# Performance work log

Measured on AMD Instinct MI355X. Metric: run time of the kernel, lower is better.

## Reference

```python
import jax, jax.numpy as jnp
import numpy as np

N_NODES = 100000
DROP_P = 0.2


def _degree_norm(idx, n):
    deg = jax.ops.segment_sum(jnp.ones_like(idx, dtype=jnp.float32), idx, num_segments=n)
    return jnp.maximum(deg, 1.0) ** -0.5


def gcn_layer(x, src, dst, W, b, n):
    # DGL GraphConv, norm='both', in_feats > out_feats so weight is applied first.
    norm_src = _degree_norm(src, n)  # out-degree^{-1/2}
    norm_dst = _degree_norm(dst, n)  # in-degree^{-1/2}
    h = (x * norm_src[:, None]) @ W            # [N, d_out]
    agg = jax.ops.segment_sum(h[src], dst, num_segments=n)  # gather-scatter over edges
    return agg * norm_dst[:, None] + b


def setup_inputs() -> dict:
    key = jax.random.key(0)
    k = jax.random.split(key, 5)
    x = jax.random.normal(k[0], (N_NODES, 256), dtype=jnp.float32)
    edge_index = jax.random.randint(k[1], (2, 1600000), 0, N_NODES, dtype=jnp.int64)
    W1 = jax.random.normal(k[2], (256, 128), dtype=jnp.float32) * (1.0 / np.sqrt(256))
    b1 = jnp.zeros((128,), dtype=jnp.float32)
    W2 = jax.random.normal(k[3], (128, 47), dtype=jnp.float32) * (1.0 / np.sqrt(128))
    b2 = jnp.zeros((47,), dtype=jnp.float32)
    return {"x": x, "edge_index": edge_index, "W1": W1, "b1": b1, "W2": W2, "b2": b2}


def reference(x, edge_index, W1, b1, W2, b2):
    src, dst = edge_index[0], edge_index[1]
    n = x.shape[0]
    # CRD: GraphConv -> relu -> dropout (F.dropout default training=True; fixed mask)
    h = gcn_layer(x, src, dst, W1, b1, n)
    h = jax.nn.relu(h)
    keep = jax.random.bernoulli(jax.random.key(42), 1.0 - DROP_P, h.shape)
    h = jnp.where(keep, h / (1.0 - DROP_P), 0.0)
    # CLS: GraphConv -> log_softmax over class dim
    out = gcn_layer(h, src, dst, W2, b2, n)
    return jax.nn.log_softmax(out, axis=-1)
```

## Files before the change

### kernel.cpp

```cpp
#include <hip/hip_runtime.h>
#include <math.h>


#define NF0 256
#define NF1 128
#define NC  47
#define CB  1024

typedef __attribute__((ext_vector_type(8))) short bfrag;
typedef __attribute__((ext_vector_type(4))) float f32x4;

__device__ __forceinline__ unsigned short f2bf(float f) {
  unsigned u = __float_as_uint(f);
  return (unsigned short)((u + 0x7fffu + ((u >> 16) & 1u)) >> 16);
}
__device__ __forceinline__ unsigned pack2bf(float a, float b) {
  return (unsigned)f2bf(a) | ((unsigned)f2bf(b) << 16);
}
__device__ __forceinline__ float bflo(unsigned v) { return __uint_as_float(v << 16); }
__device__ __forceinline__ float bfhi(unsigned v) { return __uint_as_float(v & 0xffff0000u); }
__device__ __forceinline__ float bf2f(unsigned short b) {
  return __uint_as_float((unsigned)b << 16);
}

__device__ __forceinline__ unsigned rotl_(unsigned x, int n) {
  return (x << n) | (x >> (32 - n));
}
__device__ __forceinline__ void threefry2x32_(unsigned x0, unsigned x1,
                                              unsigned& o0, unsigned& o1) {
  const unsigned k0 = 0u, k1 = 42u;
  const unsigned k2 = k0 ^ k1 ^ 0x1BD11BDAu;
  x0 += k0; x1 += k1;
  x0+=x1; x1=rotl_(x1,13); x1^=x0;
  x0+=x1; x1=rotl_(x1,15); x1^=x0;
  x0+=x1; x1=rotl_(x1,26); x1^=x0;
  x0+=x1; x1=rotl_(x1, 6); x1^=x0;
  x0+=k1; x1+=k2+1u;
  x0+=x1; x1=rotl_(x1,17); x1^=x0;
  x0+=x1; x1=rotl_(x1,29); x1^=x0;
  x0+=x1; x1=rotl_(x1,16); x1^=x0;
  x0+=x1; x1=rotl_(x1,24); x1^=x0;
  x0+=k2; x1+=k0+2u;
  x0+=x1; x1=rotl_(x1,13); x1^=x0;
  x0+=x1; x1=rotl_(x1,15); x1^=x0;
  x0+=x1; x1=rotl_(x1,26); x1^=x0;
  x0+=x1; x1=rotl_(x1, 6); x1^=x0;
  x0+=k0; x1+=k1+3u;
  x0+=x1; x1=rotl_(x1,17); x1^=x0;
  x0+=x1; x1=rotl_(x1,29); x1^=x0;
  x0+=x1; x1=rotl_(x1,16); x1^=x0;
  x0+=x1; x1=rotl_(x1,24); x1^=x0;
  x0+=k1; x1+=k2+4u;
  x0+=x1; x1=rotl_(x1,13); x1^=x0;
  x0+=x1; x1=rotl_(x1,15); x1^=x0;
  x0+=x1; x1=rotl_(x1,26); x1^=x0;
  x0+=x1; x1=rotl_(x1, 6); x1^=x0;
  x0+=k2; x1+=k0+5u;
  o0 = x0; o1 = x1;
}
__device__ __forceinline__ unsigned dropout_bit(unsigned j) {
  unsigned o0, o1;
  threefry2x32_(0u, j, o0, o1);
  unsigned bits = o0 ^ o1;
  float u = __uint_as_float((bits >> 9) | 0x3f800000u) - 1.0f;
  return (u < 0.8f) ? 1u : 0u;
}


__global__ __launch_bounds__(256) void k_chist(const int* __restrict__ ei, int E,
                                               int nbk,
                                               unsigned* __restrict__ bCntD,
                                               unsigned* __restrict__ bCntS,
                                               const float* __restrict__ W1,
                                               const float* __restrict__ W2,
                                               unsigned* __restrict__ W1t32,
                                               unsigned* __restrict__ W2t32) {
  if (blockIdx.x >= 256) {
    int i = (blockIdx.x - 256) * 256 + threadIdx.x;
    if (i < 128 * 128) {
      int n = i >> 7, k = (i & 127) << 1;
      W1t32[i] = pack2bf(W1[(size_t)k * NF1 + n], W1[(size_t)(k + 1) * NF1 + n]);
    } else if (i < 128 * 128 + 48 * 64) {
      int j = i - 128 * 128;
      int f = j >> 6, k = (j & 63) << 1;
      float a = (f < NC) ? W2[(size_t)k * NC + f] : 0.f;
      float c = (f < NC) ? W2[(size_t)(k + 1) * NC + f] : 0.f;
      W2t32[j] = pack2bf(a, c);
    }
    return;
  }
  __shared__ unsigned hd[128], hs[128];
  for (int i = threadIdx.x; i < 128; i += 256) { hd[i] = 0; hs[i] = 0; }
  __syncthreads();
  for (int e = blockIdx.x * 256 + threadIdx.x; e < E; e += 256 * 256) {
    int s = ei[e], d = ei[E + e];
    atomicAdd(&hs[s >> 10], 1u);
    atomicAdd(&hd[d >> 10], 1u);
  }
  __syncthreads();
  for (int i = threadIdx.x; i < nbk; i += 256) {
    if (hd[i]) atomicAdd(&bCntD[i], hd[i]);
    if (hs[i]) atomicAdd(&bCntS[i], hs[i]);
  }
}

__global__ __launch_bounds__(256) void k_cscatter(const int* __restrict__ ei, int E,
                                                  const unsigned* __restrict__ bCntD,
                                                  const unsigned* __restrict__ bCntS,
                                                  unsigned* __restrict__ curD,
                                                  unsigned* __restrict__ curS,
                                                  unsigned* __restrict__ pd,
                                                  unsigned short* __restrict__ ps,
                                                  int nbk) {
  __shared__ unsigned hd[128], hs[128];
  __shared__ unsigned baseD[128], baseS[128];
  __shared__ unsigned sc[256];
  const int t = threadIdx.x;
  int per = (E + gridDim.x - 1) / gridDim.x;
  int e0 = blockIdx.x * per;
  int e1 = min(e0 + per, E);
  unsigned orig = (t < 128) ? ((t < nbk) ? bCntD[t] : 0u)
                            : (((t - 128) < nbk) ? bCntS[t - 128] : 0u);
  sc[t] = orig;
  if (t < 128) { hd[t] = 0; hs[t] = 0; }
  __syncthreads();
  for (int e = e0 + t; e < e1; e += 256) {
    int s = ei[e], d = ei[E + e];
    atomicAdd(&hs[s >> 10], 1u);
    atomicAdd(&hd[d >> 10], 1u);
  }
  __syncthreads();
  #pragma unroll
  for (int o = 1; o < 128; o <<= 1) {
    unsigned u = ((t & 127) >= o) ? sc[t - o] : 0u;
    __syncthreads();
    sc[t] += u;
    __syncthreads();
  }
  if (t < 128) {
    unsigned excl = sc[t] - orig;
    unsigned h = hd[t];
    baseD[t] = excl + (h ? atomicAdd(&curD[t], h) : 0u);
    hd[t] = 0;
  } else {
    int i = t - 128;
    unsigned excl = sc[t] - orig;
    unsigned h = hs[i];
    baseS[i] = excl + (h ? atomicAdd(&curS[i], h) : 0u);
    hs[i] = 0;
  }
  __syncthreads();
  for (int e = e0 + t; e < e1; e += 256) {
    int s = ei[e], d = ei[E + e];
    int bd = d >> 10, bs = s >> 10;
    unsigned pD = baseD[bd] + atomicAdd(&hd[bd], 1u);
    unsigned pS = baseS[bs] + atomicAdd(&hs[bs], 1u);
    pd[pD] = ((unsigned)(d & (CB - 1)) << 17) | (unsigned)s;
    ps[pS] = (unsigned short)(s & (CB - 1));
  }
}

__global__ __launch_bounds__(256) void k_fine(const unsigned* __restrict__ bCntD,
                                              const unsigned* __restrict__ bCntS,
                                              const unsigned* __restrict__ pd,
                                              const unsigned short* __restrict__ ps,
                                              unsigned* __restrict__ off,
                                              float* __restrict__ norm_dst,
                                              float* __restrict__ norm_src,
                                              int* __restrict__ csr,
                                              int N, int E, int nbk,
                                              unsigned* __restrict__ bmask) {
  const int t = threadIdx.x;
  if ((int)blockIdx.x >= 2 * nbk) {
    int i = ((int)blockIdx.x - 2 * nbk) * 256 + t;
    if (i < 4 * N) {
      unsigned w = 0;
      #pragma unroll 4
      for (int tbit = 0; tbit < 32; tbit++)
        w |= dropout_bit(32u * (unsigned)i + (unsigned)tbit) << tbit;
      bmask[i] = w;
    }
    return;
  }
  __shared__ unsigned cnt[CB];
  __shared__ unsigned part[256];
  __shared__ unsigned sc[256];
  const bool isD = (int)blockIdx.x < nbk;
  const int b = isD ? (int)blockIdx.x : ((int)blockIdx.x - nbk);
  unsigned orig = (t < 128) ? ((t < nbk) ? bCntD[t] : 0u)
                            : (((t - 128) < nbk) ? bCntS[t - 128] : 0u);
  sc[t] = orig;
  __syncthreads();
  #pragma unroll
  for (int o = 1; o < 128; o <<= 1) {
    unsigned u = ((t & 127) >= o) ? sc[t - o] : 0u;
    __syncthreads();
    sc[t] += u;
    __syncthreads();
  }
  const int idx = isD ? b : (128 + b);
  const unsigned hi = sc[idx];
  const unsigned lo = hi - (isD ? bCntD[b] : bCntS[b]);
  const int base = b << 10;
  for (int i = t; i < CB; i += 256) cnt[i] = 0;
  __syncthreads();
  if (isD) {
    for (unsigned j = lo + t; j < hi; j += 256) atomicAdd(&cnt[pd[j] >> 17], 1u);
    __syncthreads();
    unsigned c0 = cnt[4*t], c1 = cnt[4*t+1], c2 = cnt[4*t+2], c3 = cnt[4*t+3];
    unsigned tsum = c0 + c1 + c2 + c3;
    part[t] = tsum;
    __syncthreads();
    #pragma unroll
    for (int o = 1; o < 256; o <<= 1) {
      unsigned u = (t >= o) ? part[t - o] : 0u;
      __syncthreads();
      part[t] += u;
      __syncthreads();
    }
    unsigned e0 = part[t] - tsum;
    unsigned p0 = e0, p1 = e0 + c0, p2 = p1 + c1, p3 = p2 + c2;
    int n0 = base + 4 * t;
    if (n0 + 0 < N) { off[n0+0] = lo + p0; norm_dst[n0+0] = 1.0f / sqrtf((float)(c0 < 1u ? 1u : c0)); }
    if (n0 + 1 < N) { off[n0+1] = lo + p1; norm_dst[n0+1] = 1.0f / sqrtf((float)(c1 < 1u ? 1u : c1)); }
    if (n0 + 2 < N) { off[n0+2] = lo + p2; norm_dst[n0+2] = 1.0f / sqrtf((float)(c2 < 1u ? 1u : c2)); }
    if (n0 + 3 < N) { off[n0+3] = lo + p3; norm_dst[n0+3] = 1.0f / sqrtf((float)(c3 < 1u ? 1u : c3)); }
    if (b == nbk - 1 && t == 0) off[N] = (unsigned)E;
    __syncthreads();
    cnt[4*t] = p0; cnt[4*t+1] = p1; cnt[4*t+2] = p2; cnt[4*t+3] = p3;
    __syncthreads();
    for (unsigned j = lo + t; j < hi; j += 256) {
      unsigned v = pd[j];
      unsigned pos = atomicAdd(&cnt[v >> 17], 1u);
      csr[lo + pos] = (int)(v & 0x1FFFFu);
    }
  } else {
    for (unsigned j = lo + t; j < hi; j += 256) atomicAdd(&cnt[ps[j]], 1u);
    __syncthreads();
    for (int i = t; i < CB; i += 256) {
      int n = base + i;
      if (n < N) {
        unsigned c = cnt[i];
        norm_src[n] = 1.0f / sqrtf((float)(c < 1u ? 1u : c));
      }
    }
  }
}

__global__ __launch_bounds__(256) void k_gemm1(const float* __restrict__ x,
                                               const unsigned* __restrict__ W1t32,
                                               const float* __restrict__ norm_src,
                                               unsigned short* __restrict__ h1, int N) {
  __shared__ unsigned As[128][20];
  __shared__ unsigned Bs[128][20];
  const int m0 = blockIdx.x * 128;
  const int t = threadIdx.x;
  const int lane = t & 63, wid = t >> 6;
  const int fr = lane & 15, ko = (lane >> 4) * 8;

  f32x4 acc[2][8];
  #pragma unroll
  for (int r = 0; r < 2; r++)
    #pragma unroll
    for (int c = 0; c < 8; c++) acc[r][c] = (f32x4){0.f, 0.f, 0.f, 0.f};

  const int sr = t >> 1;
  const int shw = (t & 1) * 8;

  for (int k0 = 0; k0 < NF0; k0 += 32) {
    {
      unsigned w[8];
      int gm = m0 + sr;
      if (gm < N) {
        const float* p = x + (size_t)gm * NF0 + k0 + shw * 2;
        #pragma unroll
        for (int q = 0; q < 4; q++) {
          float4 v = *(const float4*)(p + q * 4);
          w[2*q]   = pack2bf(v.x, v.y);
          w[2*q+1] = pack2bf(v.z, v.w);
        }
      } else {
        #pragma unroll
        for (int q = 0; q < 8; q++) w[q] = 0u;
      }
      *(uint4*)&As[sr][shw]     = make_uint4(w[0], w[1], w[2], w[3]);
      *(uint4*)&As[sr][shw + 4] = make_uint4(w[4], w[5], w[6], w[7]);
    }
    {
      const unsigned* pb = W1t32 + (size_t)sr * (NF0 / 2) + (k0 >> 1) + shw;
      *(uint4*)&Bs[sr][shw]     = *(const uint4*)pb;
      *(uint4*)&Bs[sr][shw + 4] = *(const uint4*)(pb + 4);
    }
    __syncthreads();
    const unsigned short* As16 = (const unsigned short*)&As[0][0];
    const unsigned short* Bs16 = (const unsigned short*)&Bs[0][0];
    #pragma unroll
    for (int r = 0; r < 2; r++) {
      bfrag a = *(const bfrag*)(As16 + (size_t)(wid * 32 + r * 16 + fr) * 40 + ko);
      #pragma unroll
      for (int c = 0; c < 8; c++) {
        bfrag b = *(const bfrag*)(Bs16 + (size_t)(c * 16 + fr) * 40 + ko);
        acc[r][c] = __builtin_amdgcn_mfma_f32_16x16x32_bf16(a, b, acc[r][c], 0, 0, 0);
      }
    }
    __syncthreads();
  }

  #pragma unroll
  for (int r = 0; r < 2; r++) {
    int rbase = m0 + wid * 32 + r * 16 + (lane >> 4) * 4;
    float ns[4];
    #pragma unroll
    for (int g = 0; g < 4; g++) ns[g] = (rbase + g < N) ? norm_src[rbase + g] : 0.f;
    #pragma unroll
    for (int c = 0; c < 8; c++) {
      int col = c * 16 + fr;
      #pragma unroll
      for (int g = 0; g < 4; g++) {
        int row = rbase + g;
        if (row < N) h1[(size_t)row * NF1 + col] = f2bf(acc[r][c][g] * ns[g]);
      }
    }
  }
}

__global__ __launch_bounds__(256) void k_gather1(const unsigned* __restrict__ off,
                                                 const int* __restrict__ csr,
                                                 const unsigned short* __restrict__ h1,
                                                 const float* __restrict__ norm_dst,
                                                 const float* __restrict__ norm_src,
                                                 const float* __restrict__ b1,
                                                 const unsigned* __restrict__ bmask,
                                                 unsigned* __restrict__ h2, int N) {
  const int t = threadIdx.x;
  const int lane = t & 63, wid = t >> 6;
  const int eg = lane >> 4;
  const int q  = lane & 15;
  const int ngroups = (N + 3) >> 2;
  const float4 bA = *(const float4*)(b1 + q * 8);
  const float4 bB = *(const float4*)(b1 + q * 8 + 4);

  for (int grp = blockIdx.x; grp < ngroups; grp += gridDim.x) {
    int node = grp * 4 + wid;
    if (node >= N) continue;
    unsigned j = off[node], e1 = off[node + 1];
    float ax0=0.f, ax1=0.f, ax2=0.f, ax3=0.f;
    float ay0=0.f, ay1=0.f, ay2=0.f, ay3=0.f;
    for (; j + 8 <= e1; j += 8) {
      int sA = csr[j + eg];
      int sB = csr[j + 4 + eg];
      uint4 vA = *(const uint4*)(h1 + (size_t)sA * NF1 + q * 8);
      uint4 vB = *(const uint4*)(h1 + (size_t)sB * NF1 + q * 8);
      ax0 += bflo(vA.x) + bflo(vB.x); ay0 += bfhi(vA.x) + bfhi(vB.x);
      ax1 += bflo(vA.y) + bflo(vB.y); ay1 += bfhi(vA.y) + bfhi(vB.y);
      ax2 += bflo(vA.z) + bflo(vB.z); ay2 += bfhi(vA.z) + bfhi(vB.z);
      ax3 += bflo(vA.w) + bflo(vB.w); ay3 += bfhi(vA.w) + bfhi(vB.w);
    }
    if (j + 4 <= e1) {
      int s = csr[j + eg];
      uint4 v = *(const uint4*)(h1 + (size_t)s * NF1 + q * 8);
      ax0 += bflo(v.x); ay0 += bfhi(v.x);
      ax1 += bflo(v.y); ay1 += bfhi(v.y);
      ax2 += bflo(v.z); ay2 += bfhi(v.z);
      ax3 += bflo(v.w); ay3 += bfhi(v.w);
      j += 4;
    }
    if (j < e1) {
      unsigned rem = e1 - j;
      if ((unsigned)eg < rem) {
        int s = csr[j + eg];
        uint4 v = *(const uint4*)(h1 + (size_t)s * NF1 + q * 8);
        ax0 += bflo(v.x); ay0 += bfhi(v.x);
        ax1 += bflo(v.y); ay1 += bfhi(v.y);
        ax2 += bflo(v.z); ay2 += bfhi(v.z);
        ax3 += bflo(v.w); ay3 += bfhi(v.w);
      }
    }
    ax0 += __shfl_xor(ax0, 16); ax0 += __shfl_xor(ax0, 32);
    ay0 += __shfl_xor(ay0, 16); ay0 += __shfl_xor(ay0, 32);
    ax1 += __shfl_xor(ax1, 16); ax1 += __shfl_xor(ax1, 32);
    ay1 += __shfl_xor(ay1, 16); ay1 += __shfl_xor(ay1, 32);
    ax2 += __shfl_xor(ax2, 16); ax2 += __shfl_xor(ax2, 32);
    ay2 += __shfl_xor(ay2, 16); ay2 += __shfl_xor(ay2, 32);
    ax3 += __shfl_xor(ax3, 16); ax3 += __shfl_xor(ax3, 32);
    ay3 += __shfl_xor(ay3, 16); ay3 += __shfl_xor(ay3, 32);
    if (eg == 0) {
      float nd = norm_dst[node], ns = norm_src[node];
      unsigned mw = bmask[node * 4 + (q >> 2)];
      unsigned mb = (mw >> ((q & 3) * 8)) & 0xffu;
      float v0 = fmaxf(ax0 * nd + bA.x, 0.f);
      float v1 = fmaxf(ay0 * nd + bA.y, 0.f);
      float v2 = fmaxf(ax1 * nd + bA.z, 0.f);
      float v3 = fmaxf(ay1 * nd + bA.w, 0.f);
      float v4 = fmaxf(ax2 * nd + bB.x, 0.f);
      float v5 = fmaxf(ay2 * nd + bB.y, 0.f);
      float v6 = fmaxf(ax3 * nd + bB.z, 0.f);
      float v7 = fmaxf(ay3 * nd + bB.w, 0.f);
      v0 *= ((mb >> 0) & 1 ? 1.25f : 0.f) * ns;
      v1 *= ((mb >> 1) & 1 ? 1.25f : 0.f) * ns;
      v2 *= ((mb >> 2) & 1 ? 1.25f : 0.f) * ns;
      v3 *= ((mb >> 3) & 1 ? 1.25f : 0.f) * ns;
      v4 *= ((mb >> 4) & 1 ? 1.25f : 0.f) * ns;
      v5 *= ((mb >> 5) & 1 ? 1.25f : 0.f) * ns;
      v6 *= ((mb >> 6) & 1 ? 1.25f : 0.f) * ns;
      v7 *= ((mb >> 7) & 1 ? 1.25f : 0.f) * ns;
      uint4 o;
      o.x = pack2bf(v0, v1);
      o.y = pack2bf(v2, v3);
      o.z = pack2bf(v4, v5);
      o.w = pack2bf(v6, v7);
      *(uint4*)(h2 + (size_t)node * 64 + q * 4) = o;
    }
  }
}

__global__ __launch_bounds__(256) void k_gemm2(const unsigned* __restrict__ h2,
                                               const unsigned* __restrict__ W2t32,
                                               unsigned short* __restrict__ g, int N) {
  const int t = threadIdx.x;
  const int lane = t & 63, wid = t >> 6;
  const int fr = lane & 15, hi4 = lane >> 4;
  const int row = blockIdx.x * 64 + wid * 16 + fr;

  bfrag a[4];
  const unsigned* ap = h2 + (size_t)row * 64 + hi4 * 4;
  #pragma unroll
  for (int kk = 0; kk < 4; kk++) {
    uint4 v = *(const uint4*)(ap + kk * 16);
    a[kk] = *(bfrag*)&v;
  }

  const int rbase = blockIdx.x * 64 + wid * 16 + hi4 * 4;
  #pragma unroll
  for (int c = 0; c < 3; c++) {
    f32x4 acc = (f32x4){0.f, 0.f, 0.f, 0.f};
    const unsigned* bp = W2t32 + (size_t)(c * 16 + fr) * 64 + hi4 * 4;
    #pragma unroll
    for (int kk = 0; kk < 4; kk++) {
      uint4 w = *(const uint4*)(bp + kk * 16);
      bfrag b = *(bfrag*)&w;
      acc = __builtin_amdgcn_mfma_f32_16x16x32_bf16(a[kk], b, acc, 0, 0, 0);
    }
    int col = c * 16 + fr;
    #pragma unroll
    for (int r = 0; r < 4; r++) {
      int nr = rbase + r;
      if (nr < N) g[(size_t)nr * 64 + col] = f2bf(acc[r]);
    }
  }
  #pragma unroll
  for (int r = 0; r < 4; r++) {
    int nr = rbase + r;
    if (nr < N) g[(size_t)nr * 64 + 48 + fr] = 0;
  }
}

__global__ __launch_bounds__(256) void k_gather2(const unsigned* __restrict__ off,
                                                 const int* __restrict__ csr,
                                                 const unsigned* __restrict__ g64,
                                                 const float* __restrict__ norm_dst,
                                                 const float* __restrict__ b2,
                                                 float* __restrict__ out, int N) {
  int node = (blockIdx.x * 256 + threadIdx.x) >> 6;
  int lane = threadIdx.x & 63;
  if (node >= N) return;
  const int h = lane >> 5, q = lane & 31;
  unsigned j = off[node], e1 = off[node + 1];
  float a0 = 0.f, a1 = 0.f;
  for (; j + 4 <= e1; j += 4) {
    int sA = csr[j + h], sB = csr[j + 2 + h];
    unsigned vA = g64[(size_t)sA * 32 + q];
    unsigned vB = g64[(size_t)sB * 32 + q];
    a0 += bflo(vA) + bflo(vB);
    a1 += bfhi(vA) + bfhi(vB);
  }
  if (j + 2 <= e1) {
    int s = csr[j + h];
    unsigned v = g64[(size_t)s * 32 + q];
    a0 += bflo(v); a1 += bfhi(v);
    j += 2;
  }
  if (j < e1 && h == 0) {
    int s = csr[j];
    unsigned v = g64[(size_t)s * 32 + q];
    a0 += bflo(v); a1 += bfhi(v);
  }
  a0 += __shfl_xor(a0, 32);
  a1 += __shfl_xor(a1, 32);
  float nd = norm_dst[node];
  int f0 = 2 * q, f1 = 2 * q + 1;
  float v0 = (f0 < NC) ? a0 * nd + b2[f0] : -INFINITY;
  float v1 = (f1 < NC) ? a1 * nd + b2[f1] : -INFINITY;
  float m = fmaxf(v0, v1);
  #pragma unroll
  for (int o = 16; o; o >>= 1) m = fmaxf(m, __shfl_xor(m, o));
  float ex = ((f0 < NC) ? expf(v0 - m) : 0.f) + ((f1 < NC) ? expf(v1 - m) : 0.f);
  #pragma unroll
  for (int o = 16; o; o >>= 1) ex += __shfl_xor(ex, o);
  float ls = logf(ex);
  if (h == 0) {
    if (f0 < NC) out[(size_t)node * NC + f0] = v0 - m - ls;
    if (f1 < NC) out[(size_t)node * NC + f1] = v1 - m - ls;
  }
}

extern "C" void kernel_launch(void* const* d_in, const int* in_sizes, int n_in,
                              void* d_out, int out_size, void* d_ws, size_t ws_size,
                              hipStream_t stream) {
  const float* x  = (const float*)d_in[0];
  const int*   ei = (const int*)d_in[1];
  const float* W1 = (const float*)d_in[2];
  const float* b1 = (const float*)d_in[3];
  const float* W2 = (const float*)d_in[4];
  const float* b2 = (const float*)d_in[5];
  float* out = (float*)d_out;

  const int N = in_sizes[0] / NF0;
  const int E = in_sizes[1] / 2;
  const int nbk = (N + CB - 1) / CB;
  const int Npad = (N + 63) & ~63;

  unsigned* ws = (unsigned*)d_ws;
  size_t o = 0;
  auto alloc = [&](size_t elems) { size_t p = o; o += (elems + 3) & ~(size_t)3; return p; };
  float*    norm_src = (float*)(ws + alloc(N));
  float*    norm_dst = (float*)(ws + alloc(N));
  unsigned* off      = ws + alloc(N + 1);
  unsigned* bCntD    = ws + alloc(128);
  unsigned* bCntS    = ws + alloc(128);
  unsigned* curD     = ws + alloc(128);
  unsigned* curS     = ws + alloc(128);
  unsigned* bmask    = ws + alloc((size_t)4 * N);
  unsigned* pd       = ws + alloc(E);
  unsigned short* ps = (unsigned short*)(ws + alloc(E / 2));
  int*      csr      = (int*)(ws + alloc(E));
  unsigned* W1t32    = ws + alloc(128 * 128);
  unsigned* W2t32    = ws + alloc(48 * 64);
  unsigned short* h1 = (unsigned short*)(ws + alloc((size_t)N * NF1 / 2));
  unsigned* h2       = ws + alloc((size_t)Npad * 64);
  unsigned short* g64 = h1;

  hipMemsetAsync(bCntD, 0, 512 * sizeof(unsigned), stream);

  int wblk = (128 * 128 + 48 * 64 + 255) / 256;
  int mblk = (4 * N + 255) / 256;
  k_chist<<<256 + wblk, 256, 0, stream>>>(ei, E, nbk, bCntD, bCntS, W1, W2,
                                          W1t32, W2t32);
  k_cscatter<<<256, 256, 0, stream>>>(ei, E, bCntD, bCntS, curD, curS, pd, ps, nbk);
  k_fine<<<2 * nbk + mblk, 256, 0, stream>>>(bCntD, bCntS, pd, ps, off, norm_dst,
                                             norm_src, csr, N, E, nbk, bmask);
  k_gemm1<<<(N + 127) / 128, 256, 0, stream>>>(x, W1t32, norm_src, h1, N);
  k_gather1<<<2048, 256, 0, stream>>>(off, csr, h1, norm_dst, norm_src, b1, bmask,
                                      h2, N);
  k_gemm2<<<Npad / 64, 256, 0, stream>>>(h2, W2t32, g64, N);
  k_gather2<<<((size_t)N * 64 + 255) / 256, 256, 0, stream>>>(
      off, csr, (const unsigned*)g64, norm_dst, b2, out, N);
}
```

Before: 457.6 us.

## Fuse layer-2 GEMM into gather1 epilogue via per-wave MFMA on 16 nodes

Each wave in gather1 now aggregates 16 consecutive nodes, shuffles the bf16 activations into MFMA A-fragments, and multiplies them by W2 directly. This writes g64 itself and removes the k_gemm2 launch along with the h2 round trip through global memory. Because g64 can no longer alias h1 while h1 is still being read, it gets its own buffer. Gather2's inner loop is also unrolled to 8 edges for more memory-level parallelism. The trade-offs are 16 serial node iterations per wave, a fixed grid instead of the grid-stride loop, and extra shuffles per node.

```diff
diff --git a/kernel.cpp b/kernel.cpp
--- a/kernel.cpp
+++ b/kernel.cpp
@@ -331,18 +331,27 @@
                                                  const float* __restrict__ norm_src,
                                                  const float* __restrict__ b1,
                                                  const unsigned* __restrict__ bmask,
-                                                 unsigned* __restrict__ h2, int N) {
+                                                 const unsigned* __restrict__ W2t32,
+                                                 unsigned short* __restrict__ g64,
+                                                 int N) {
   const int t = threadIdx.x;
   const int lane = t & 63, wid = t >> 6;
   const int eg = lane >> 4;
   const int q  = lane & 15;
-  const int ngroups = (N + 3) >> 2;
   const float4 bA = *(const float4*)(b1 + q * 8);
   const float4 bB = *(const float4*)(b1 + q * 8 + 4);
 
-  for (int grp = blockIdx.x; grp < ngroups; grp += gridDim.x) {
-    int node = grp * 4 + wid;
-    if (node >= N) continue;
+  const int wbase = (blockIdx.x * 4 + wid) * 16;
+  if (wbase >= N) return;
+
+  uint4 af[4];
+  #pragma unroll
+  for (int kk = 0; kk < 4; kk++) af[kk] = make_uint4(0u, 0u, 0u, 0u);
+
+  #pragma unroll 1
+  for (int i = 0; i < 16; i++) {
+    const int node = wbase + i;
+    if (node >= N) break;
     unsigned j = off[node], e1 = off[node + 1];
     float ax0=0.f, ax1=0.f, ax2=0.f, ax3=0.f;
     float ay0=0.f, ay1=0.f, ay2=0.f, ay3=0.f;
@@ -384,74 +393,62 @@
     ay2 += __shfl_xor(ay2, 16); ay2 += __shfl_xor(ay2, 32);
     ax3 += __shfl_xor(ax3, 16); ax3 += __shfl_xor(ax3, 32);
     ay3 += __shfl_xor(ay3, 16); ay3 += __shfl_xor(ay3, 32);
-    if (eg == 0) {
-      float nd = norm_dst[node], ns = norm_src[node];
-      unsigned mw = bmask[node * 4 + (q >> 2)];
-      unsigned mb = (mw >> ((q & 3) * 8)) & 0xffu;
-      float v0 = fmaxf(ax0 * nd + bA.x, 0.f);
-      float v1 = fmaxf(ay0 * nd + bA.y, 0.f);
-      float v2 = fmaxf(ax1 * nd + bA.z, 0.f);
-      float v3 = fmaxf(ay1 * nd + bA.w, 0.f);
-      float v4 = fmaxf(ax2 * nd + bB.x, 0.f);
-      float v5 = fmaxf(ay2 * nd + bB.y, 0.f);
-      float v6 = fmaxf(ax3 * nd + bB.z, 0.f);
-      float v7 = fmaxf(ay3 * nd + bB.w, 0.f);
-      v0 *= ((mb >> 0) & 1 ? 1.25f : 0.f) * ns;
-      v1 *= ((mb >> 1) & 1 ? 1.25f : 0.f) * ns;
-      v2 *= ((mb >> 2) & 1 ? 1.25f : 0.f) * ns;
-      v3 *= ((mb >> 3) & 1 ? 1.25f : 0.f) * ns;
-      v4 *= ((mb >> 4) & 1 ? 1.25f : 0.f) * ns;
-      v5 *= ((mb >> 5) & 1 ? 1.25f : 0.f) * ns;
-      v6 *= ((mb >> 6) & 1 ? 1.25f : 0.f) * ns;
-      v7 *= ((mb >> 7) & 1 ? 1.25f : 0.f) * ns;
-      uint4 o;
-      o.x = pack2bf(v0, v1);
-      o.y = pack2bf(v2, v3);
-      o.z = pack2bf(v4, v5);
-      o.w = pack2bf(v6, v7);
-      *(uint4*)(h2 + (size_t)node * 64 + q * 4) = o;
-    }
-  }
-}
-
-__global__ __launch_bounds__(256) void k_gemm2(const unsigned* __restrict__ h2,
-                                               const unsigned* __restrict__ W2t32,
-                                               unsigned short* __restrict__ g, int N) {
-  const int t = threadIdx.x;
-  const int lane = t & 63, wid = t >> 6;
-  const int fr = lane & 15, hi4 = lane >> 4;
-  const int row = blockIdx.x * 64 + wid * 16 + fr;
-
-  bfrag a[4];
-  const unsigned* ap = h2 + (size_t)row * 64 + hi4 * 4;
-  #pragma unroll
-  for (int kk = 0; kk < 4; kk++) {
-    uint4 v = *(const uint4*)(ap + kk * 16);
-    a[kk] = *(bfrag*)&v;
-  }
-
-  const int rbase = blockIdx.x * 64 + wid * 16 + hi4 * 4;
+    float nd = norm_dst[node], ns = norm_src[node];
+    unsigned mw = bmask[node * 4 + (q >> 2)];
+    unsigned mb = (mw >> ((q & 3) * 8)) & 0xffu;
+    float v0 = fmaxf(ax0 * nd + bA.x, 0.f);
+    float v1 = fmaxf(ay0 * nd + bA.y, 0.f);
+    float v2 = fmaxf(ax1 * nd + bA.z, 0.f);
+    float v3 = fmaxf(ay1 * nd + bA.w, 0.f);
+    float v4 = fmaxf(ax2 * nd + bB.x, 0.f);
+    float v5 = fmaxf(ay2 * nd + bB.y, 0.f);
+    float v6 = fmaxf(ax3 * nd + bB.z, 0.f);
+    float v7 = fmaxf(ay3 * nd + bB.w, 0.f);
+    v0 *= ((mb >> 0) & 1 ? 1.25f : 0.f) * ns;
+    v1 *= ((mb >> 1) & 1 ? 1.25f : 0.f) * ns;
+    v2 *= ((mb >> 2) & 1 ? 1.25f : 0.f) * ns;
+    v3 *= ((mb >> 3) & 1 ? 1.25f : 0.f) * ns;
+    v4 *= ((mb >> 4) & 1 ? 1.25f : 0.f) * ns;
+    v5 *= ((mb >> 5) & 1 ? 1.25f : 0.f) * ns;
+    v6 *= ((mb >> 6) & 1 ? 1.25f : 0.f) * ns;
+    v7 *= ((mb >> 7) & 1 ? 1.25f : 0.f) * ns;
+    uint4 o;
+    o.x = pack2bf(v0, v1);
+    o.y = pack2bf(v2, v3);
+    o.z = pack2bf(v4, v5);
+    o.w = pack2bf(v6, v7);
+    #pragma unroll
+    for (int kk = 0; kk < 4; kk++) {
+      int srcl = 4 * kk + eg;
+      unsigned t0 = __shfl(o.x, srcl);
+      unsigned t1 = __shfl(o.y, srcl);
+      unsigned t2 = __shfl(o.z, srcl);
+      unsigned t3 = __shfl(o.w, srcl);
+      if (q == i) af[kk] = make_uint4(t0, t1, t2, t3);
+    }
+  }
+
   #pragma unroll
   for (int c = 0; c < 3; c++) {
     f32x4 acc = (f32x4){0.f, 0.f, 0.f, 0.f};
-    const unsigned* bp = W2t32 + (size_t)(c * 16 + fr) * 64 + hi4 * 4;
+    const unsigned* bp = W2t32 + (size_t)(c * 16 + q) * 64 + eg * 4;
     #pragma unroll
     for (int kk = 0; kk < 4; kk++) {
       uint4 w = *(const uint4*)(bp + kk * 16);
-      bfrag b = *(bfrag*)&w;
-      acc = __builtin_amdgcn_mfma_f32_16x16x32_bf16(a[kk], b, acc, 0, 0, 0);
-    }
-    int col = c * 16 + fr;
+      acc = __builtin_amdgcn_mfma_f32_16x16x32_bf16(*(bfrag*)&af[kk], *(bfrag*)&w,
+                                                    acc, 0, 0, 0);
+    }
+    int col = c * 16 + q;
     #pragma unroll
     for (int r = 0; r < 4; r++) {
-      int nr = rbase + r;
-      if (nr < N) g[(size_t)nr * 64 + col] = f2bf(acc[r]);
+      int nr = wbase + eg * 4 + r;
+      if (nr < N) g64[(size_t)nr * 64 + col] = f2bf(acc[r]);
     }
   }
   #pragma unroll
   for (int r = 0; r < 4; r++) {
-    int nr = rbase + r;
-    if (nr < N) g[(size_t)nr * 64 + 48 + fr] = 0;
+    int nr = wbase + eg * 4 + r;
+    if (nr < N) g64[(size_t)nr * 64 + 48 + q] = 0;
   }
 }
 
@@ -467,12 +464,23 @@
   const int h = lane >> 5, q = lane & 31;
   unsigned j = off[node], e1 = off[node + 1];
   float a0 = 0.f, a1 = 0.f;
-  for (; j + 4 <= e1; j += 4) {
+  for (; j + 8 <= e1; j += 8) {
+    int s0 = csr[j + h],     s1 = csr[j + 2 + h];
+    int s2 = csr[j + 4 + h], s3 = csr[j + 6 + h];
+    unsigned v0 = g64[(size_t)s0 * 32 + q];
+    unsigned v1 = g64[(size_t)s1 * 32 + q];
+    unsigned v2 = g64[(size_t)s2 * 32 + q];
+    unsigned v3 = g64[(size_t)s3 * 32 + q];
+    a0 += (bflo(v0) + bflo(v1)) + (bflo(v2) + bflo(v3));
+    a1 += (bfhi(v0) + bfhi(v1)) + (bfhi(v2) + bfhi(v3));
+  }
+  if (j + 4 <= e1) {
     int sA = csr[j + h], sB = csr[j + 2 + h];
     unsigned vA = g64[(size_t)sA * 32 + q];
     unsigned vB = g64[(size_t)sB * 32 + q];
     a0 += bflo(vA) + bflo(vB);
     a1 += bfhi(vA) + bfhi(vB);
+    j += 4;
   }
   if (j + 2 <= e1) {
     int s = csr[j + h];
@@ -537,8 +545,8 @@
   unsigned* W1t32    = ws + alloc(128 * 128);
   unsigned* W2t32    = ws + alloc(48 * 64);
   unsigned short* h1 = (unsigned short*)(ws + alloc((size_t)N * NF1 / 2));
-  unsigned* h2       = ws + alloc((size_t)Npad * 64);
-  unsigned short* g64 = h1;
+  unsigned* g64u     = ws + alloc((size_t)Npad * 32);
+  unsigned short* g64 = (unsigned short*)g64u;
 
   hipMemsetAsync(bCntD, 0, 512 * sizeof(unsigned), stream);
 
@@ -550,9 +558,8 @@
   k_fine<<<2 * nbk + mblk, 256, 0, stream>>>(bCntD, bCntS, pd, ps, off, norm_dst,
                                              norm_src, csr, N, E, nbk, bmask);
   k_gemm1<<<(N + 127) / 128, 256, 0, stream>>>(x, W1t32, norm_src, h1, N);
-  k_gather1<<<2048, 256, 0, stream>>>(off, csr, h1, norm_dst, norm_src, b1, bmask,
-                                      h2, N);
-  k_gemm2<<<Npad / 64, 256, 0, stream>>>(h2, W2t32, g64, N);
+  k_gather1<<<(N + 63) / 64, 256, 0, stream>>>(off, csr, h1, norm_dst, norm_src,
+                                               b1, bmask, W2t32, g64, N);
   k_gather2<<<((size_t)N * 64 + 255) / 256, 256, 0, stream>>>(
-      off, csr, (const unsigned*)g64, norm_dst, b2, out, N);
-}
+      off, csr, (const unsigned*)g64u, norm_dst, b2, out, N);
+}
```

Result: faster. 436.2 us (-4.7%).
